# Kernel optimization log

Measured on AMD Instinct MI355X. Metric: run time of the kernel, lower is better.

## Reference

```python
import jax, jax.numpy as jnp
import numpy as np

B, L, D, H, I = 4, 1024, 2048, 16, 8192
DH = D // H  # 128
EPS = 1e-6


def setup_inputs() -> dict:
    key = jax.random.key(0)
    ks = jax.random.split(key, 10)
    hidden_states = jax.random.normal(ks[0], (B, L, D), dtype=jnp.float32)
    # additive causal mask [B,1,L,L]: 0 on allowed, large negative on masked
    causal = jnp.tril(jnp.ones((L, L), dtype=bool))
    attention_mask = jnp.where(causal, 0.0, -1e9).astype(jnp.float32)
    attention_mask = jnp.broadcast_to(attention_mask[None, None], (B, 1, L, L))
    # RoPE tables [B,L,DH]
    inv_freq = 1.0 / (10000.0 ** (jnp.arange(0, DH, 2, dtype=jnp.float32) / DH))
    pos = jnp.arange(L, dtype=jnp.float32)
    freqs = pos[:, None] * inv_freq[None, :]            # [L, DH/2]
    emb = jnp.concatenate([freqs, freqs], axis=-1)       # [L, DH]
    cos = jnp.broadcast_to(jnp.cos(emb)[None], (B, L, DH)).astype(jnp.float32)
    sin = jnp.broadcast_to(jnp.sin(emb)[None], (B, L, DH)).astype(jnp.float32)
    s = 0.02
    return {
        "hidden_states": hidden_states,
        "attention_mask": attention_mask,
        "cos": cos,
        "sin": sin,
        "q_w": jax.random.normal(ks[1], (D, D), jnp.float32) * s,
        "k_w": jax.random.normal(ks[2], (D, D), jnp.float32) * s,
        "v_w": jax.random.normal(ks[3], (D, D), jnp.float32) * s,
        "o_w": jax.random.normal(ks[4], (D, D), jnp.float32) * s,
        "gate_w": jax.random.normal(ks[5], (I, D), jnp.float32) * s,
        "up_w": jax.random.normal(ks[6], (I, D), jnp.float32) * s,
        "down_w": jax.random.normal(ks[7], (D, I), jnp.float32) * s,
        "ln1_w": jnp.ones((D,), jnp.float32),
        "ln2_w": jnp.ones((D,), jnp.float32),
    }


def _rms_norm(x, w):
    var = jnp.mean(jnp.square(x), axis=-1, keepdims=True)
    return x * jax.lax.rsqrt(var + EPS) * w


def _rotate_half(x):
    x1, x2 = jnp.split(x, 2, axis=-1)
    return jnp.concatenate([-x2, x1], axis=-1)


def reference(hidden_states, attention_mask, cos, sin, q_w, k_w, v_w, o_w,
              gate_w, up_w, down_w, ln1_w, ln2_w):
    residual = hidden_states
    h = _rms_norm(hidden_states, ln1_w)                       # [B,L,D]
    # QKV projections (torch Linear: x @ W^T)
    def heads(x, w):
        return (x @ w.T).reshape(B, L, H, DH).transpose(0, 2, 1, 3)  # [B,H,L,DH]
    q, k, v = heads(h, q_w), heads(h, k_w), heads(h, v_w)
    cos_b, sin_b = cos[:, None], sin[:, None]                 # [B,1,L,DH]
    q = q * cos_b + _rotate_half(q) * sin_b
    k = k * cos_b + _rotate_half(k) * sin_b
    scores = jnp.einsum('bhqd,bhkd->bhqk', q, k) / jnp.sqrt(jnp.float32(DH))
    scores = scores + attention_mask                          # [B,H,L,L]
    attn = jax.nn.softmax(scores, axis=-1)
    ctx = jnp.einsum('bhqk,bhkd->bhqd', attn, v)              # [B,H,L,DH]
    ctx = ctx.transpose(0, 2, 1, 3).reshape(B, L, D)
    attn_out = ctx @ o_w.T
    h1 = residual + attn_out
    h2 = _rms_norm(h1, ln2_w)
    mlp = (jax.nn.silu(h2 @ gate_w.T) * (h2 @ up_w.T)) @ down_w.T
    out = h1 + mlp
    return out, attn
```

## Files before the change

kernel.cpp:

```cpp
#include <hip/hip_runtime.h>


typedef __bf16 bf16;
typedef __bf16 bf16x8 __attribute__((ext_vector_type(8)));
typedef __bf16 bf16x4 __attribute__((ext_vector_type(4)));
typedef float  f32x4  __attribute__((ext_vector_type(4)));

constexpr int   kB  = 4;
constexpr int   kL  = 1024;
constexpr int   kD  = 2048;
constexpr int   kH  = 16;
constexpr int   kI  = 8192;
constexpr int   kDH = 128;
constexpr int   kQKV = 3 * kD;
constexpr float kEps = 1e-6f;
constexpr float kScoreScale = 0.08838834764831845f;

typedef __attribute__((address_space(1))) void gvoid_t;
typedef __attribute__((address_space(3))) void lvoid_t;

__device__ __forceinline__ void gload_lds16(const void* g, void* l) {
  __builtin_amdgcn_global_load_lds((gvoid_t*)g, (lvoid_t*)l, 16, 0, 0);
}

__global__ __launch_bounds__(256) void cast_f32_bf16_kernel(
    const float* __restrict__ x, bf16* __restrict__ y, long n) {
  long i = ((long)blockIdx.x * 256 + threadIdx.x) * 4;
  long stride = (long)gridDim.x * 256 * 4;
  for (; i < n; i += stride) {
    const float4 v = *reinterpret_cast<const float4*>(x + i);
    bf16x4 o;
    o[0] = (bf16)v.x; o[1] = (bf16)v.y; o[2] = (bf16)v.z; o[3] = (bf16)v.w;
    *reinterpret_cast<bf16x4*>(y + i) = o;
  }
}

__global__ __launch_bounds__(256) void rmsnorm_kernel(
    const float* __restrict__ x, const float* __restrict__ w,
    bf16* __restrict__ out) {
  const long row = blockIdx.x;
  const float* xr = x + row * (long)kD;
  bf16* orow = out + row * (long)kD;
  const int t = threadIdx.x;

  float4 v0 = *(const float4*)(xr + t * 8);
  float4 v1 = *(const float4*)(xr + t * 8 + 4);
  float ss = v0.x * v0.x + v0.y * v0.y + v0.z * v0.z + v0.w * v0.w +
             v1.x * v1.x + v1.y * v1.y + v1.z * v1.z + v1.w * v1.w;

  __shared__ float red[4];
  for (int off = 32; off > 0; off >>= 1) ss += __shfl_down(ss, off);
  if ((t & 63) == 0) red[t >> 6] = ss;
  __syncthreads();
  const float tot = red[0] + red[1] + red[2] + red[3];
  const float rs = rsqrtf(tot / (float)kD + kEps);

  float4 w0 = *(const float4*)(w + t * 8);
  float4 w1 = *(const float4*)(w + t * 8 + 4);
  bf16x8 o;
  o[0] = (bf16)(v0.x * rs * w0.x); o[1] = (bf16)(v0.y * rs * w0.y);
  o[2] = (bf16)(v0.z * rs * w0.z); o[3] = (bf16)(v0.w * rs * w0.w);
  o[4] = (bf16)(v1.x * rs * w1.x); o[5] = (bf16)(v1.y * rs * w1.y);
  o[6] = (bf16)(v1.z * rs * w1.z); o[7] = (bf16)(v1.w * rs * w1.w);
  *(bf16x8*)(orow + t * 8) = o;
}

__global__ __launch_bounds__(256) void rope_kernel(
    bf16* __restrict__ qkv, const float* __restrict__ cosb,
    const float* __restrict__ sinb) {
  const long row = blockIdx.x;
  const float* cr = cosb + row * (long)kDH;
  const float* sr = sinb + row * (long)kDH;
  bf16* qr = qkv + row * (long)kQKV;
  bf16* kr = qr + kD;
  const int t = threadIdx.x;
#pragma unroll
  for (int it = 0; it < 4; ++it) {
    const int p = it * 256 + t;
    const int h = p >> 6, i = p & 63;
    const int i0 = h * kDH + i, i1 = i0 + 64;
    const float c0 = cr[i], s0 = sr[i], c1 = cr[i + 64], s1 = sr[i + 64];
    const float q0 = (float)qr[i0], q1 = (float)qr[i1];
    qr[i0] = (bf16)(q0 * c0 - q1 * s0);
    qr[i1] = (bf16)(q1 * c1 + q0 * s1);
    const float k0 = (float)kr[i0], k1 = (float)kr[i1];
    kr[i0] = (bf16)(k0 * c0 - k1 * s0);
    kr[i1] = (bf16)(k1 * c1 + k0 * s1);
  }
}

__global__ __launch_bounds__(256) void transpose_v_kernel(
    const bf16* __restrict__ qkv, bf16* __restrict__ vT) {
  __shared__ bf16 tile[32][33];
  const int z = blockIdx.z, b = z / kH, h = z % kH;
  const bf16* src = qkv + (long)b * kL * kQKV + 2 * kD + h * kDH;
  bf16* dst = vT + (long)z * kDH * kL;
  const int l0 = blockIdx.x * 32, d0 = blockIdx.y * 32;
  const int tx = threadIdx.x & 31, ty = threadIdx.x >> 5;
  for (int r = ty; r < 32; r += 8)
    tile[r][tx] = src[(long)(l0 + r) * kQKV + d0 + tx];
  __syncthreads();
  for (int r = ty; r < 32; r += 8)
    dst[(long)(d0 + r) * kL + l0 + tx] = tile[tx][r];
}

__global__ __launch_bounds__(256) void softmax_kernel(float* __restrict__ attn) {
  const long row = blockIdx.x;
  float* r = attn + row * (long)kL;
  const int t = threadIdx.x;
  float4 v = *(float4*)(r + t * 4);

  __shared__ float red[4];
  float m = fmaxf(fmaxf(v.x, v.y), fmaxf(v.z, v.w));
  for (int off = 32; off > 0; off >>= 1) m = fmaxf(m, __shfl_down(m, off));
  if ((t & 63) == 0) red[t >> 6] = m;
  __syncthreads();
  m = fmaxf(fmaxf(red[0], red[1]), fmaxf(red[2], red[3]));

  v.x = expf(v.x - m); v.y = expf(v.y - m);
  v.z = expf(v.z - m); v.w = expf(v.w - m);
  float s = v.x + v.y + v.z + v.w;
  __syncthreads();
  for (int off = 32; off > 0; off >>= 1) s += __shfl_down(s, off);
  if ((t & 63) == 0) red[t >> 6] = s;
  __syncthreads();
  s = red[0] + red[1] + red[2] + red[3];
  const float inv = 1.0f / s;
  v.x *= inv; v.y *= inv; v.z *= inv; v.w *= inv;
  *(float4*)(r + t * 4) = v;
}

enum { EPI_NONE = 0, EPI_ADD = 1, EPI_MASK = 2, EPI_SILU = 3, EPI_OUTADD = 4 };

template <typename OutT, int EPI, bool AF32, int NF>
__device__ __forceinline__ void gemm_body(
    const void* __restrict__ Ap, long sAo, long sAi, int lda,
    const bf16* __restrict__ Bp, long sBo, long sBi, int ldb,
    OutT* Cp, long sCo, long sCi, int ldc,
    const void* Ep, long sEo, long sEi, int lde,
    float scale, int Hdiv, int M, int N, int K) {
  constexpr int BN = 32 * NF;
  constexpr int ACH = 512;
  constexpr int BCH = BN * 4;

  const int z = blockIdx.z;
  const int zo = z / Hdiv, zi = z % Hdiv;

  const bf16* A = nullptr;
  const float* Af = nullptr;
  if constexpr (AF32) Af = (const float*)Ap + zo * sAo + zi * sAi;
  else                A  = (const bf16*)Ap + zo * sAo + zi * sAi;
  const bf16* Bw = Bp + zo * sBo + zi * sBi;
  OutT* C = Cp + zo * sCo + zi * sCi;

  __shared__ __align__(16) bf16 lsA[2][128 * 32];
  __shared__ __align__(16) bf16 lsB[2][BN * 32];

  const int t = threadIdx.x;
  const int m0 = blockIdx.y * 128, n0 = blockIdx.x * BN;
  const int wave = t >> 6, lane = t & 63;
  const int wm = (wave >> 1) * 64, wn = (wave & 1) * (NF * 16);
  const int lr = lane & 15, lg = lane >> 4;

  f32x4 acc[4][NF] = {};

  auto stage = [&](int buf, int k0) {
    if constexpr (AF32) {
#pragma unroll
      for (int c = 0; c < 2; ++c) {
        const int id = c * 256 + t;
        const int row = id >> 2, col = (id & 3) * 8;
        const float* src = Af + (long)(m0 + row) * lda + k0 + col;
        const float4 u0 = *(const float4*)src;
        const float4 u1 = *(const float4*)(src + 4);
        bf16x8 wv;
        wv[0] = (bf16)u0.x; wv[1] = (bf16)u0.y; wv[2] = (bf16)u0.z; wv[3] = (bf16)u0.w;
        wv[4] = (bf16)u1.x; wv[5] = (bf16)u1.y; wv[6] = (bf16)u1.z; wv[7] = (bf16)u1.w;
        *(bf16x8*)&lsA[buf][id * 8] = wv;
        if (NF == 4 || c == 0)
          gload_lds16(Bw + (long)(n0 + row) * ldb + k0 + col, &lsB[buf][id * 8]);
      }
    } else {
#pragma unroll
      for (int c = 0; c < (ACH + BCH) / 256; ++c) {
        const int id = c * 256 + t;
        if (id < ACH) {
          const int row = id >> 2, col = (id & 3) * 8;
          gload_lds16(A + (long)(m0 + row) * lda + k0 + col, &lsA[buf][id * 8]);
        } else {
          const int fid = id - ACH;
          const int row = fid >> 2, col = (fid & 3) * 8;
          gload_lds16(Bw + (long)(n0 + row) * ldb + k0 + col, &lsB[buf][fid * 8]);
        }
      }
    }
  };

  auto compute = [&](int buf) {
    bf16x8 af[4], bfr[NF];
#pragma unroll
    for (int i = 0; i < 4; ++i)
      af[i] = *(const bf16x8*)&lsA[buf][(wm + i * 16 + lr) * 32 + lg * 8];
#pragma unroll
    for (int j = 0; j < NF; ++j)
      bfr[j] = *(const bf16x8*)&lsB[buf][(wn + j * 16 + lr) * 32 + lg * 8];
#pragma unroll
    for (int i = 0; i < 4; ++i)
#pragma unroll
      for (int j = 0; j < NF; ++j)
        acc[i][j] = __builtin_amdgcn_mfma_f32_16x16x32_bf16(af[i], bfr[j],
                                                            acc[i][j], 0, 0, 0);
  };

  stage(0, 0);
  __syncthreads();

  int cur = 0;
  for (int k0 = 0; k0 < K - 32; k0 += 32) {
    stage(cur ^ 1, k0 + 32);
    compute(cur);
    __syncthreads();
    cur ^= 1;
  }
  compute(cur);

  const float* Ef = (const float*)Ep;
  const bf16* Eb = (const bf16*)Ep;
  long ebase = 0;
  if constexpr (EPI == EPI_ADD || EPI == EPI_SILU)
    ebase = zo * sEo + zi * sEi;
#pragma unroll
  for (int i = 0; i < 4; ++i) {
#pragma unroll
    for (int j = 0; j < NF; ++j) {
      const int col = n0 + wn + j * 16 + lr;
#pragma unroll
      for (int r = 0; r < 4; ++r) {
        const int rowi = m0 + wm + i * 16 + lg * 4 + r;
        float val = acc[i][j][r] * scale;
        const long idx = (long)rowi * ldc + col;
        if constexpr (EPI == EPI_MASK) {
          if (col > rowi) val += -1.0e9f;
        }
        if constexpr (EPI == EPI_ADD) {
          val += Ef[ebase + (long)rowi * lde + col];
        }
        if constexpr (EPI == EPI_SILU) {
          const float g = (float)Eb[ebase + (long)rowi * lde + col];
          val = (g / (1.0f + expf(-g))) * val;
        }
        if constexpr (EPI == EPI_OUTADD)
          val += ((float*)Cp)[zo * sCo + zi * sCi + idx];
        C[idx] = (OutT)val;
      }
    }
  }
}

#define GEMM_ARGS                                                        \
  const void* __restrict__ Ap, long sAo, long sAi, int lda,              \
  const bf16* __restrict__ Bp, long sBo, long sBi, int ldb,              \
  void* Cp, long sCo, long sCi, int ldc,                                 \
  const void* Ep, long sEo, long sEi, int lde,                           \
  float scale, int Hdiv, int M, int N, int K
#define GEMM_PASS Ap, sAo, sAi, lda, Bp, sBo, sBi, ldb, (OUT_T*)Cp, sCo, \
  sCi, ldc, Ep, sEo, sEi, lde, scale, Hdiv, M, N, K

#define DEF_GEMM(NAME, OUT_TY, EPI_V, AF32_V, NF_V)                      \
  __global__ __launch_bounds__(256) void NAME(GEMM_ARGS) {               \
    using OUT_T = OUT_TY;                                                \
    gemm_body<OUT_T, EPI_V, AF32_V, NF_V>(GEMM_PASS);                    \
  }

DEF_GEMM(gemm_qkv,    bf16,  EPI_NONE,   false, 4)
DEF_GEMM(gemm_scores, float, EPI_MASK,   false, 4)
DEF_GEMM(gemm_ctx,    bf16,  EPI_NONE,   true,  2)
DEF_GEMM(gemm_oproj,  float, EPI_ADD,    false, 2)
DEF_GEMM(gemm_gate,   bf16,  EPI_NONE,   false, 4)
DEF_GEMM(gemm_up,     bf16,  EPI_SILU,   false, 4)
DEF_GEMM(gemm_down,   float, EPI_OUTADD, false, 2)

extern "C" void kernel_launch(void* const* d_in, const int* in_sizes, int n_in,
                              void* d_out, int out_size, void* d_ws,
                              size_t ws_size, hipStream_t stream) {
  (void)in_sizes; (void)n_in; (void)out_size; (void)ws_size;

  const float* hidden = (const float*)d_in[0];
  const float* cosb   = (const float*)d_in[2];
  const float* sinb   = (const float*)d_in[3];
  const float* q_w    = (const float*)d_in[4];
  const float* k_w    = (const float*)d_in[5];
  const float* v_w    = (const float*)d_in[6];
  const float* o_w    = (const float*)d_in[7];
  const float* gate_w = (const float*)d_in[8];
  const float* up_w   = (const float*)d_in[9];
  const float* down_w = (const float*)d_in[10];
  const float* ln1    = (const float*)d_in[11];
  const float* ln2    = (const float*)d_in[12];

  float* out  = (float*)d_out;
  float* attn = out + (long)kB * kL * kD;

  bf16* wsb = (bf16*)d_ws;
  long off = 0;
  bf16* WQKV = wsb + off; off += 3L * kD * kD;
  bf16* WO   = wsb + off; off += (long)kD * kD;
  bf16* WBIG = wsb + off; off += (long)kI * kD;
  bf16* HBF  = wsb + off; off += (long)kB * kL * kD;
  bf16* QKV  = wsb + off; off += (long)kB * kL * kQKV;
  bf16* GBUF = wsb + off; off += (long)kB * kL * kI;

  const long DD = (long)kD * kD;
  const long ID = (long)kI * kD;
  const int  ML = kB * kL;

  cast_f32_bf16_kernel<<<dim3((int)(DD / 1024)), 256, 0, stream>>>(q_w, WQKV, DD);
  cast_f32_bf16_kernel<<<dim3((int)(DD / 1024)), 256, 0, stream>>>(k_w, WQKV + DD, DD);
  cast_f32_bf16_kernel<<<dim3((int)(DD / 1024)), 256, 0, stream>>>(v_w, WQKV + 2 * DD, DD);
  cast_f32_bf16_kernel<<<dim3((int)(DD / 1024)), 256, 0, stream>>>(o_w, WO, DD);

  rmsnorm_kernel<<<ML, 256, 0, stream>>>(hidden, ln1, HBF);

  gemm_qkv<<<dim3(kQKV / 128, ML / 128, 1), 256, 0, stream>>>(
      HBF, 0, 0, kD, WQKV, 0, 0, kD, QKV, 0, 0, kQKV,
      nullptr, 0, 0, 0, 1.0f, 1, ML, kQKV, kD);

  rope_kernel<<<ML, 256, 0, stream>>>(QKV, cosb, sinb);

  transpose_v_kernel<<<dim3(kL / 32, kDH / 32, kB * kH), 256, 0, stream>>>(QKV, GBUF);

  gemm_scores<<<dim3(kL / 128, kL / 128, kB * kH), 256, 0, stream>>>(
      QKV, (long)kL * kQKV, kDH, kQKV,
      QKV + kD, (long)kL * kQKV, kDH, kQKV,
      attn, (long)kH * kL * kL, (long)kL * kL, kL,
      nullptr, 0, 0, 0,
      kScoreScale, kH, kL, kL, kDH);

  softmax_kernel<<<kB * kH * kL, 256, 0, stream>>>(attn);

  gemm_ctx<<<dim3(kDH / 64, kL / 128, kB * kH), 256, 0, stream>>>(
      attn, (long)kH * kL * kL, (long)kL * kL, kL,
      GBUF, (long)kH * kDH * kL, (long)kDH * kL, kL,
      HBF, (long)kL * kD, kDH, kD,
      nullptr, 0, 0, 0, 1.0f, kH, kL, kDH, kL);

  gemm_oproj<<<dim3(kD / 64, ML / 128, 1), 256, 0, stream>>>(
      HBF, 0, 0, kD, WO, 0, 0, kD, out, 0, 0, kD,
      hidden, 0, 0, kD, 1.0f, 1, ML, kD, kD);

  bf16* H2 = QKV;
  rmsnorm_kernel<<<ML, 256, 0, stream>>>(out, ln2, H2);

  cast_f32_bf16_kernel<<<dim3((int)(ID / 1024)), 256, 0, stream>>>(gate_w, WBIG, ID);
  gemm_gate<<<dim3(kI / 128, ML / 128, 1), 256, 0, stream>>>(
      H2, 0, 0, kD, WBIG, 0, 0, kD, GBUF, 0, 0, kI,
      nullptr, 0, 0, 0, 1.0f, 1, ML, kI, kD);

  cast_f32_bf16_kernel<<<dim3((int)(ID / 1024)), 256, 0, stream>>>(up_w, WBIG, ID);
  gemm_up<<<dim3(kI / 128, ML / 128, 1), 256, 0, stream>>>(
      H2, 0, 0, kD, WBIG, 0, 0, kD, GBUF, 0, 0, kI,
      GBUF, 0, 0, kI, 1.0f, 1, ML, kI, kD);

  cast_f32_bf16_kernel<<<dim3((int)(ID / 1024)), 256, 0, stream>>>(down_w, WBIG, ID);
  gemm_down<<<dim3(kD / 64, ML / 128, 1), 256, 0, stream>>>(
      GBUF, 0, 0, kI, WBIG, 0, 0, kI, out, 0, 0, kD,
      nullptr, 0, 0, 0, 1.0f, 1, ML, kD, kI);
}
```

Before: 1.148 ms.

## Two-pass causal softmax via recompute, skip masked tiles, split-K down proj

Replaces the scores GEMM plus separate softmax with two score GEMM passes. The first pass writes per-tile row max/sum stats and skips fully masked tiles, a small kernel merges the stats, and the second pass recomputes the scores, writes normalized probabilities and zero-fills the masked tiles. This removes the fp32 read-modify-write of the full attention matrix, at the cost of doing the QK^T GEMM twice. The context GEMM limits K to the causal extent, and the down projection is split along K across two z-slices, with a partial buffer and an extra add kernel to raise parallelism.

```diff
diff --git a/kernel.cpp b/kernel.cpp
--- a/kernel.cpp
+++ b/kernel.cpp
@@ -32,6 +32,18 @@
     bf16x4 o;
     o[0] = (bf16)v.x; o[1] = (bf16)v.y; o[2] = (bf16)v.z; o[3] = (bf16)v.w;
     *reinterpret_cast<bf16x4*>(y + i) = o;
+  }
+}
+
+__global__ __launch_bounds__(256) void add_inplace_kernel(
+    float* __restrict__ o, const float* __restrict__ p, long n) {
+  long i = ((long)blockIdx.x * 256 + threadIdx.x) * 4;
+  const long stride = (long)gridDim.x * 1024;
+  for (; i < n; i += stride) {
+    float4 a = *(float4*)(o + i);
+    const float4 b = *(const float4*)(p + i);
+    a.x += b.x; a.y += b.y; a.z += b.z; a.w += b.w;
+    *(float4*)(o + i) = a;
   }
 }
 
@@ -104,35 +116,23 @@
     dst[(long)(d0 + r) * kL + l0 + tx] = tile[tx][r];
 }
 
-__global__ __launch_bounds__(256) void softmax_kernel(float* __restrict__ attn) {
-  const long row = blockIdx.x;
-  float* r = attn + row * (long)kL;
-  const int t = threadIdx.x;
-  float4 v = *(float4*)(r + t * 4);
-
-  __shared__ float red[4];
-  float m = fmaxf(fmaxf(v.x, v.y), fmaxf(v.z, v.w));
-  for (int off = 32; off > 0; off >>= 1) m = fmaxf(m, __shfl_down(m, off));
-  if ((t & 63) == 0) red[t >> 6] = m;
-  __syncthreads();
-  m = fmaxf(fmaxf(red[0], red[1]), fmaxf(red[2], red[3]));
-
-  v.x = expf(v.x - m); v.y = expf(v.y - m);
-  v.z = expf(v.z - m); v.w = expf(v.w - m);
-  float s = v.x + v.y + v.z + v.w;
-  __syncthreads();
-  for (int off = 32; off > 0; off >>= 1) s += __shfl_down(s, off);
-  if ((t & 63) == 0) red[t >> 6] = s;
-  __syncthreads();
-  s = red[0] + red[1] + red[2] + red[3];
-  const float inv = 1.0f / s;
-  v.x *= inv; v.y *= inv; v.z *= inv; v.w *= inv;
-  *(float4*)(r + t * 4) = v;
-}
-
-enum { EPI_NONE = 0, EPI_ADD = 1, EPI_MASK = 2, EPI_SILU = 3, EPI_OUTADD = 4 };
-
-template <typename OutT, int EPI, bool AF32, int NF>
+__global__ __launch_bounds__(256) void merge_stats_kernel(
+    const float2* __restrict__ sp, float2* __restrict__ sm) {
+  const int idx = blockIdx.x * 256 + threadIdx.x;
+  const int row = idx & 1023;
+  const int n = ((row >> 7) + 1) * 2;
+  const float2* p = sp + ((long)idx << 4);
+  float M = -3.0e38f;
+  for (int i = 0; i < n; ++i) M = fmaxf(M, p[i].x);
+  float S = 0.f;
+  for (int i = 0; i < n; ++i) S += p[i].y * expf(p[i].x - M);
+  sm[idx] = make_float2(M, 1.0f / S);
+}
+
+enum { EPI_NONE = 0, EPI_ADD = 1, EPI_SILU = 3, EPI_SPLIT = 5,
+       EPI_PASS1 = 6, EPI_PASS2 = 7 };
+
+template <typename OutT, int EPI, bool AF32, int NF, bool CK>
 __device__ __forceinline__ void gemm_body(
     const void* __restrict__ Ap, long sAo, long sAi, int lda,
     const bf16* __restrict__ Bp, long sBo, long sBi, int ldb,
@@ -142,6 +142,7 @@
   constexpr int BN = 32 * NF;
   constexpr int ACH = 512;
   constexpr int BCH = BN * 4;
+  static_assert((EPI != EPI_PASS1 && EPI != EPI_PASS2) || NF == 4, "pass NF=4");
 
   const int z = blockIdx.z;
   const int zo = z / Hdiv, zi = z % Hdiv;
@@ -153,11 +154,26 @@
   const bf16* Bw = Bp + zo * sBo + zi * sBi;
   OutT* C = Cp + zo * sCo + zi * sCi;
 
+  const int t = threadIdx.x;
+  const int m0 = blockIdx.y * 128, n0 = blockIdx.x * BN;
+
+  if constexpr (EPI == EPI_PASS1) {
+    if (blockIdx.x > blockIdx.y) return;
+  }
+  if constexpr (EPI == EPI_PASS2) {
+    if (blockIdx.x > blockIdx.y) {
+      for (int e = t; e < 128 * 32; e += 256) {
+        const int row = e >> 5, col = (e & 31) * 4;
+        *(float4*)&C[(long)(m0 + row) * ldc + n0 + col] =
+            make_float4(0.f, 0.f, 0.f, 0.f);
+      }
+      return;
+    }
+  }
+
   __shared__ __align__(16) bf16 lsA[2][128 * 32];
   __shared__ __align__(16) bf16 lsB[2][BN * 32];
 
-  const int t = threadIdx.x;
-  const int m0 = blockIdx.y * 128, n0 = blockIdx.x * BN;
   const int wave = t >> 6, lane = t & 63;
   const int wm = (wave >> 1) * 64, wn = (wave & 1) * (NF * 16);
   const int lr = lane & 15, lg = lane >> 4;
@@ -212,11 +228,12 @@
                                                             acc[i][j], 0, 0, 0);
   };
 
+  const int Klim = CK ? (m0 + 128) : K;
+
   stage(0, 0);
   __syncthreads();
-
   int cur = 0;
-  for (int k0 = 0; k0 < K - 32; k0 += 32) {
+  for (int k0 = 0; k0 < Klim - 32; k0 += 32) {
     stage(cur ^ 1, k0 + 32);
     compute(cur);
     __syncthreads();
@@ -224,34 +241,80 @@
   }
   compute(cur);
 
-  const float* Ef = (const float*)Ep;
-  const bf16* Eb = (const bf16*)Ep;
-  long ebase = 0;
-  if constexpr (EPI == EPI_ADD || EPI == EPI_SILU)
-    ebase = zo * sEo + zi * sEi;
-#pragma unroll
-  for (int i = 0; i < 4; ++i) {
-#pragma unroll
-    for (int j = 0; j < NF; ++j) {
-      const int col = n0 + wn + j * 16 + lr;
+  if constexpr (EPI == EPI_PASS1) {
+    float2* statsP = (float2*)Ep;
+    const int half = wn >> 6, nt = blockIdx.x;
+#pragma unroll
+    for (int i = 0; i < 4; ++i) {
 #pragma unroll
       for (int r = 0; r < 4; ++r) {
-        const int rowi = m0 + wm + i * 16 + lg * 4 + r;
-        float val = acc[i][j][r] * scale;
-        const long idx = (long)rowi * ldc + col;
-        if constexpr (EPI == EPI_MASK) {
-          if (col > rowi) val += -1.0e9f;
+        const int rowg = m0 + wm + i * 16 + lg * 4 + r;
+        float v[NF];
+        float mx = -3.0e38f;
+#pragma unroll
+        for (int j = 0; j < NF; ++j) {
+          const int colg = n0 + wn + j * 16 + lr;
+          v[j] = acc[i][j][r] * scale + (colg > rowg ? -1.0e9f : 0.0f);
+          mx = fmaxf(mx, v[j]);
         }
-        if constexpr (EPI == EPI_ADD) {
-          val += Ef[ebase + (long)rowi * lde + col];
+        for (int sh = 1; sh <= 8; sh <<= 1) mx = fmaxf(mx, __shfl_xor(mx, sh));
+        float s = 0.f;
+#pragma unroll
+        for (int j = 0; j < NF; ++j) s += expf(v[j] - mx);
+        for (int sh = 1; sh <= 8; sh <<= 1) s += __shfl_xor(s, sh);
+        if (lr == 0)
+          statsP[(((long)(z << 10) + rowg) << 4) + nt * 2 + half] =
+              make_float2(mx, s);
+      }
+    }
+  } else if constexpr (EPI == EPI_PASS2) {
+    const float2* sm = (const float2*)Ep;
+#pragma unroll
+    for (int i = 0; i < 4; ++i) {
+#pragma unroll
+      for (int j = 0; j < NF; ++j) {
+        const int colg = n0 + wn + j * 16 + lr;
+#pragma unroll
+        for (int r = 0; r < 4; ++r) {
+          const int rowg = m0 + wm + i * 16 + lg * 4 + r;
+          float p = 0.0f;
+          if (colg <= rowg) {
+            const float2 st = sm[(z << 10) + rowg];
+            p = expf(acc[i][j][r] * scale - st.x) * st.y;
+          }
+          C[(long)rowg * ldc + colg] = (OutT)p;
         }
-        if constexpr (EPI == EPI_SILU) {
-          const float g = (float)Eb[ebase + (long)rowi * lde + col];
-          val = (g / (1.0f + expf(-g))) * val;
+      }
+    }
+  } else {
+    const float* Ef = (const float*)Ep;
+    const bf16* Eb = (const bf16*)Ep;
+    long ebase = 0;
+    if constexpr (EPI == EPI_ADD || EPI == EPI_SILU)
+      ebase = zo * sEo + zi * sEi;
+#pragma unroll
+    for (int i = 0; i < 4; ++i) {
+#pragma unroll
+      for (int j = 0; j < NF; ++j) {
+        const int col = n0 + wn + j * 16 + lr;
+#pragma unroll
+        for (int r = 0; r < 4; ++r) {
+          const int rowi = m0 + wm + i * 16 + lg * 4 + r;
+          float val = acc[i][j][r] * scale;
+          const long idx = (long)rowi * ldc + col;
+          if constexpr (EPI == EPI_SPLIT) {
+            if (zo == 0) C[idx] = val + C[idx];
+            else         ((float*)Ep)[idx] = val;
+          } else {
+            if constexpr (EPI == EPI_ADD)
+              val += Ef[ebase + (long)rowi * lde + col];
+            if constexpr (EPI == EPI_SILU) {
+              const float g = (float)Eb[ebase + (long)rowi * lde + col];
+              val = (g / (1.0f + expf(-g))) * val;
+            }
+            C[idx] = (OutT)val;
+          }
         }
-        if constexpr (EPI == EPI_OUTADD)
-          val += ((float*)Cp)[zo * sCo + zi * sCi + idx];
-        C[idx] = (OutT)val;
       }
     }
   }
@@ -266,19 +329,20 @@
 #define GEMM_PASS Ap, sAo, sAi, lda, Bp, sBo, sBi, ldb, (OUT_T*)Cp, sCo, \
   sCi, ldc, Ep, sEo, sEi, lde, scale, Hdiv, M, N, K
 
-#define DEF_GEMM(NAME, OUT_TY, EPI_V, AF32_V, NF_V)                      \
+#define DEF_GEMM(NAME, OUT_TY, EPI_V, AF32_V, NF_V, CK_V)                \
   __global__ __launch_bounds__(256) void NAME(GEMM_ARGS) {               \
     using OUT_T = OUT_TY;                                                \
-    gemm_body<OUT_T, EPI_V, AF32_V, NF_V>(GEMM_PASS);                    \
-  }
-
-DEF_GEMM(gemm_qkv,    bf16,  EPI_NONE,   false, 4)
-DEF_GEMM(gemm_scores, float, EPI_MASK,   false, 4)
-DEF_GEMM(gemm_ctx,    bf16,  EPI_NONE,   true,  2)
-DEF_GEMM(gemm_oproj,  float, EPI_ADD,    false, 2)
-DEF_GEMM(gemm_gate,   bf16,  EPI_NONE,   false, 4)
-DEF_GEMM(gemm_up,     bf16,  EPI_SILU,   false, 4)
-DEF_GEMM(gemm_down,   float, EPI_OUTADD, false, 2)
+    gemm_body<OUT_T, EPI_V, AF32_V, NF_V, CK_V>(GEMM_PASS);              \
+  }
+
+DEF_GEMM(gemm_qkv,   bf16,  EPI_NONE,  false, 4, false)
+DEF_GEMM(gemm_sc1,   float, EPI_PASS1, false, 4, false)
+DEF_GEMM(gemm_sc2,   float, EPI_PASS2, false, 4, false)
+DEF_GEMM(gemm_ctx,   bf16,  EPI_NONE,  true,  2, true)
+DEF_GEMM(gemm_oproj, float, EPI_ADD,   false, 2, false)
+DEF_GEMM(gemm_gate,  bf16,  EPI_NONE,  false, 4, false)
+DEF_GEMM(gemm_up,    bf16,  EPI_SILU,  false, 4, false)
+DEF_GEMM(gemm_downs, float, EPI_SPLIT, false, 2, false)
 
 extern "C" void kernel_launch(void* const* d_in, const int* in_sizes, int n_in,
                               void* d_out, int out_size, void* d_ws,
@@ -310,6 +374,10 @@
   bf16* QKV  = wsb + off; off += (long)kB * kL * kQKV;
   bf16* GBUF = wsb + off; off += (long)kB * kL * kI;
 
+  float2* STATS_P = (float2*)HBF;
+  float2* STATS_M = STATS_P + (64L * 1024 * 16);
+  float* DPART = (float*)(QKV + (long)kB * kL * kD);
+
   const long DD = (long)kD * kD;
   const long ID = (long)kI * kD;
   const int  ML = kB * kL;
@@ -329,14 +397,21 @@
 
   transpose_v_kernel<<<dim3(kL / 32, kDH / 32, kB * kH), 256, 0, stream>>>(QKV, GBUF);
 
-  gemm_scores<<<dim3(kL / 128, kL / 128, kB * kH), 256, 0, stream>>>(
+  gemm_sc1<<<dim3(kL / 128, kL / 128, kB * kH), 256, 0, stream>>>(
       QKV, (long)kL * kQKV, kDH, kQKV,
       QKV + kD, (long)kL * kQKV, kDH, kQKV,
       attn, (long)kH * kL * kL, (long)kL * kL, kL,
-      nullptr, 0, 0, 0,
+      STATS_P, 0, 0, 0,
       kScoreScale, kH, kL, kL, kDH);
 
-  softmax_kernel<<<kB * kH * kL, 256, 0, stream>>>(attn);
+  merge_stats_kernel<<<256, 256, 0, stream>>>(STATS_P, STATS_M);
+
+  gemm_sc2<<<dim3(kL / 128, kL / 128, kB * kH), 256, 0, stream>>>(
+      QKV, (long)kL * kQKV, kDH, kQKV,
+      QKV + kD, (long)kL * kQKV, kDH, kQKV,
+      attn, (long)kH * kL * kL, (long)kL * kL, kL,
+      STATS_M, 0, 0, 0,
+      kScoreScale, kH, kL, kL, kDH);
 
   gemm_ctx<<<dim3(kDH / 64, kL / 128, kB * kH), 256, 0, stream>>>(
       attn, (long)kH * kL * kL, (long)kL * kL, kL,
@@ -362,7 +437,9 @@
       GBUF, 0, 0, kI, 1.0f, 1, ML, kI, kD);
 
   cast_f32_bf16_kernel<<<dim3((int)(ID / 1024)), 256, 0, stream>>>(down_w, WBIG, ID);
-  gemm_down<<<dim3(kD / 64, ML / 128, 1), 256, 0, stream>>>(
-      GBUF, 0, 0, kI, WBIG, 0, 0, kI, out, 0, 0, kD,
-      nullptr, 0, 0, 0, 1.0f, 1, ML, kD, kI);
-}
+  gemm_downs<<<dim3(kD / 64, ML / 128, 2), 256, 0, stream>>>(
+      GBUF, 4096, 0, kI, WBIG, 4096, 0, kI, out, 0, 0, kD,
+      DPART, 0, 0, kD, 1.0f, 1, ML, kD, kI / 2);
+
+  add_inplace_kernel<<<2048, 256, 0, stream>>>(out, DPART, (long)ML * kD);
+}
```

After: 1.195 ms. 4.1% more time.
